# Performance work log

Hardware: AMD Instinct MI355X
Metric: run time of the kernel (lower is better)

The kernel has to match this reference:

```python
import jax, jax.numpy as jnp
import numpy as np

DEPTH = 2
DIM = 512
FF = 2048
INNER = 32
VOCAB = 8192
B = 2
L = 512
LN_EPS = 1e-5


def _layer_norm(x, g, b):
    m = jnp.mean(x, axis=-1, keepdims=True)
    v = jnp.var(x, axis=-1, keepdims=True)
    return (x - m) * jax.lax.rsqrt(v + LN_EPS) * g + b


def _sioconv_layer(x, wa, wx, v_re, v_im, h0_re, h0_im, w_ol):
    # x: [B, L, DIM] float32
    Bb, Ll, _ = x.shape
    I = v_re.shape[0]
    # complex gate a with magnitude sigmoid(log|a|^2)
    af = (x @ wa.T).reshape(Bb, Ll, I, 2)
    a = jax.lax.complex(af[..., 0], af[..., 1])
    m = jnp.square(af[..., 0]) + jnp.square(af[..., 1])
    a = a * jax.lax.rsqrt(m) * jax.nn.sigmoid(jnp.log(m))  # [B,L,I] complex
    # complex input x with magnitude |x| (x * rsqrt(|x|^2) * |x|^2)
    xf = (x @ wx.T).reshape(Bb, Ll, I, 2)
    xc = jax.lax.complex(xf[..., 0], xf[..., 1])
    mx = jnp.square(xf[..., 0]) + jnp.square(xf[..., 1])
    xc = xc * jax.lax.rsqrt(mx) * mx  # [B,L,I] complex
    # cumulative log-decay products: the original's FFT conv of the upper-
    # triangular a_ln against an all-ones matrix is exactly a cumsum along j.
    a_ln = jnp.log(a)  # [B,L,I]
    ii = jnp.arange(Ll)[:, None]
    jj = jnp.arange(Ll)[None, :]
    tri = jnp.where((jj >= ii)[None, None, :, :],
                    jnp.transpose(a_ln, (0, 2, 1))[:, :, None, :],
                    jnp.zeros((), a_ln.dtype))  # [B,I,L,L]: tri[b,d,i,j]=a_ln[b,j,d] for j>=i
    s = jnp.cumsum(tri, axis=3)
    # c[b,d,i,j] = prod_{t=i..j} a[b,t,d] for j>=i; =1 at j=i-1; 0 below.
    c = jnp.where((jj >= ii - 1)[None, None, :, :], jnp.exp(s), jnp.zeros((), s.dtype))
    V = jax.lax.complex(v_re, v_im)
    Vinv = jnp.linalg.inv(V)
    h0 = jax.lax.complex(h0_re, h0_im)  # [I]
    xct = jnp.transpose(xc, (0, 2, 1))  # [B,I,L]
    x_roll = jnp.roll(xct, 1, axis=2).at[:, :, 0].set(h0[None, :])
    # original builds C[b,l,m,n,o] = V diag(c) V^-1 then einsum; contract lazily:
    y = jnp.einsum('ko,bol->bkl', Vinv, x_roll)  # eigenbasis inputs [B,I,L]
    t = jnp.einsum('bkij,bki->bjk', c, y)        # recurrence in eigenbasis [B,L,I]
    h = jnp.einsum('bjk,nk->bjn', t, V)          # back to state basis [B,L,I]
    h = h.at[:, -1, :].add(xc[:, -1, :])         # last step input (others already in c via j=i-1 band)
    return jnp.real(h) @ w_ol.T


def setup_inputs() -> dict:
    key = jax.random.key(0)
    ks = jax.random.split(key, 16)
    f = lambda k, shp: jax.random.normal(k, shp, dtype=jnp.float32)
    return {
        'x': f(ks[0], (B, L, VOCAB)),
        'w_in': f(ks[1], (DIM, VOCAB)) * VOCAB ** -0.5,
        'b_in': jnp.zeros((DIM,), jnp.float32),
        'ln1_g': jnp.ones((DEPTH, DIM), jnp.float32),
        'ln1_b': jnp.zeros((DEPTH, DIM), jnp.float32),
        'wa': f(ks[2], (DEPTH, 2 * INNER, DIM)) * DIM ** -0.5,
        'wx': f(ks[3], (DEPTH, 2 * INNER, DIM)) * DIM ** -0.5,
        'v_re': f(ks[4], (DEPTH, INNER, INNER)),
        'v_im': f(ks[5], (DEPTH, INNER, INNER)),
        'h0_re': f(ks[6], (DEPTH, INNER)),
        'h0_im': f(ks[7], (DEPTH, INNER)),
        'w_ol': f(ks[8], (DEPTH, DIM, INNER)) * INNER ** -0.5,
        'ln2_g': jnp.ones((DEPTH, DIM), jnp.float32),
        'ln2_b': jnp.zeros((DEPTH, DIM), jnp.float32),
        'w1': f(ks[9], (DEPTH, FF, DIM)) * DIM ** -0.5,
        'b1': jnp.zeros((DEPTH, FF), jnp.float32),
        'w2': f(ks[10], (DEPTH, DIM, FF)) * FF ** -0.5,
        'b2': jnp.zeros((DEPTH, DIM), jnp.float32),
        'lnl_g': jnp.ones((DIM,), jnp.float32),
        'lnl_b': jnp.zeros((DIM,), jnp.float32),
        'w_out': f(ks[11], (VOCAB, DIM)) * DIM ** -0.5,
        'b_out': jnp.zeros((VOCAB,), jnp.float32),
    }


def reference(x, w_in, b_in, ln1_g, ln1_b, wa, wx, v_re, v_im, h0_re, h0_im,
              w_ol, ln2_g, ln2_b, w1, b1, w2, b2, lnl_g, lnl_b, w_out, b_out):
    h = x @ w_in.T + b_in  # [B,L,DIM]
    for d in range(DEPTH):
        r = h
        z = _layer_norm(h, ln1_g[d], ln1_b[d])
        z = _sioconv_layer(z, wa[d], wx[d], v_re[d], v_im[d], h0_re[d], h0_im[d], w_ol[d])
        h = z + r
        r = h
        z = _layer_norm(h, ln2_g[d], ln2_b[d])
        z = jax.nn.silu(z @ w1[d].T + b1[d]) @ w2[d].T + b2[d]
        h = z + r
    h = _layer_norm(h, lnl_g, lnl_b)
    return h @ w_out.T + b_out
```

## Files before the change

### kernel.cpp

```cpp
#include <hip/hip_runtime.h>
#include <stdint.h>

#define DEPTHC 2
#define DIMC   512
#define FFC    2048
#define INNERC 32
#define VOCABC 8192
#define BC     2
#define LC     512
#define NTOK   1024

typedef _Float16 f16;
typedef __attribute__((ext_vector_type(8))) _Float16 f16x8;
typedef __attribute__((ext_vector_type(4))) float f32x4;

__device__ __forceinline__ float2 cmul2(float2 a, float2 b){
    return make_float2(a.x*b.x - a.y*b.y, a.x*b.y + a.y*b.x);
}
__device__ __forceinline__ float2 cadd2(float2 a, float2 b){
    return make_float2(a.x + b.x, a.y + b.y);
}

__device__ __forceinline__ void gl_lds16(const void* g, void* l){
    __builtin_amdgcn_global_load_lds(
        (const __attribute__((address_space(1))) unsigned int*)g,
        (__attribute__((address_space(3))) unsigned int*)l, 16, 0, 0);
}

__global__ __launch_bounds__(256) void k_prep(
    const float* __restrict__ s0, const float* __restrict__ s1,
    const float* __restrict__ s2, const float* __restrict__ s3,
    const float* __restrict__ s4,
    f16* __restrict__ d0, f16* __restrict__ d1, f16* __restrict__ d2,
    f16* __restrict__ d3, f16* __restrict__ d4,
    int n0, int n1, int n2, int n3, int n4,
    const float* __restrict__ v_re, const float* __restrict__ v_im,
    const float* __restrict__ h0re, const float* __restrict__ h0im,
    float2* __restrict__ vinv, float2* __restrict__ h0c)
{
    __shared__ float2 M[32][64];
    if (blockIdx.x < 2){
        const int d = blockIdx.x;
        const int tid = threadIdx.x;
        const int c = tid & 63;
        const int wv = tid >> 6;
        if (tid < 32) h0c[d*32 + tid] = make_float2(h0re[d*32 + tid], h0im[d*32 + tid]);
#pragma unroll
        for (int rr = 0; rr < 8; ++rr){
            int r = wv*8 + rr;
            float re, im;
            if (c < 32){ re = v_re[d*1024 + r*32 + c]; im = v_im[d*1024 + r*32 + c]; }
            else       { re = (c - 32 == r) ? 1.f : 0.f; im = 0.f; }
            M[r][c] = make_float2(re, im);
        }
        __syncthreads();
#pragma unroll 1
        for (int col = 0; col < 32; ++col){
            float2 prow = M[col][c];
            float pvx = __shfl(prow.x, col, 64);
            float pvy = __shfl(prow.y, col, 64);
            float dm = pvx*pvx + pvy*pvy;
            float ir = pvx/dm, ii = -pvy/dm;
            float2 nv = make_float2(prow.x*ir - prow.y*ii, prow.x*ii + prow.y*ir);
#pragma unroll
            for (int rr = 0; rr < 8; ++rr){
                int r = wv*8 + rr;
                if (r == col) continue;
                float2 f  = M[r][col];
                float2 m0 = M[r][c];
                m0.x -= f.x*nv.x - f.y*nv.y;
                m0.y -= f.x*nv.y + f.y*nv.x;
                M[r][c] = m0;
            }
            __syncthreads();
        }
        if (c >= 32){
#pragma unroll
            for (int rr = 0; rr < 8; ++rr){
                int r = wv*8 + rr;
                float2 dv = M[r][r];
                float dm = dv.x*dv.x + dv.y*dv.y;
                float ir = dv.x/dm, ii = -dv.y/dm;
                float2 m0 = M[r][c];
                vinv[d*1024 + r*32 + (c - 32)] =
                    make_float2(m0.x*ir - m0.y*ii, m0.x*ii + m0.y*ir);
            }
        }
        return;
    }
    long long i = ((long long)(blockIdx.x - 2) * 256 + threadIdx.x) * 4;
    const float* s; f16* d;
    if (i < n0){ s = s0; d = d0; }
    else { i -= n0;
        if (i < n1){ s = s1; d = d1; }
        else { i -= n1;
            if (i < n2){ s = s2; d = d2; }
            else { i -= n2;
                if (i < n3){ s = s3; d = d3; }
                else { i -= n3; if (i >= n4) return; s = s4; d = d4; }
            }
        }
    }
    float4 v = *(const float4*)(s + i);
    union { f16 h[4]; float2 f2; } u;
    u.h[0] = (f16)v.x; u.h[1] = (f16)v.y; u.h[2] = (f16)v.z; u.h[3] = (f16)v.w;
    *(float2*)(d + i) = u.f2;
}

template<int MT, int NT, int MODE>
__global__ __launch_bounds__(256) void k_gemmT(
    const f16* __restrict__ A, const f16* __restrict__ Bw,
    void* __restrict__ C, const float* __restrict__ bias,
    int N, int K, int klen, int partStride)
{
    constexpr int RM = MT/32, RN = NT/32;
    __shared__ __align__(16) f16 As[MT*32];
    __shared__ __align__(16) f16 Bs[NT*32];
    const int tid = threadIdx.x;
    const int m0 = blockIdx.y * MT;
    const int n0 = blockIdx.x * NT;
    const int kbeg = blockIdx.z * klen;
    const int l = tid & 63;
    const int w = tid >> 6;
    const int fr = l & 15;
    const int fq = l >> 4;
    const int wm = (w >> 1) * (MT/2);
    const int wn = (w & 1) * (NT/2);
    const f16* gA = A  + (size_t)(m0 + (tid >> 2)) * K + kbeg + (tid & 3) * 8;
    const f16* gB = Bw + (size_t)(n0 + (tid >> 2)) * K + kbeg + (tid & 3) * 8;
    const size_t rowskip = (size_t)64 * K;
    f16* lA = As + tid * 8;
    f16* lB = Bs + tid * 8;
    f32x4 acc[RM][RN];
#pragma unroll
    for (int i = 0; i < RM; ++i)
#pragma unroll
        for (int j = 0; j < RN; ++j)
            acc[i][j] = (f32x4){0.f, 0.f, 0.f, 0.f};
    for (int kk = 0; kk < klen; kk += 32){
        __syncthreads();
#pragma unroll
        for (int i = 0; i < MT/64; ++i) gl_lds16(gA + i*rowskip, lA + i*2048);
#pragma unroll
        for (int i = 0; i < NT/64; ++i) gl_lds16(gB + i*rowskip, lB + i*2048);
        gA += 32; gB += 32;
        __syncthreads();
        f16x8 af[RM], bf[RN];
#pragma unroll
        for (int i = 0; i < RM; ++i) af[i] = *(const f16x8*)(As + (wm + 16*i + fr) * 32 + fq * 8);
#pragma unroll
        for (int j = 0; j < RN; ++j) bf[j] = *(const f16x8*)(Bs + (wn + 16*j + fr) * 32 + fq * 8);
#pragma unroll
        for (int i = 0; i < RM; ++i)
#pragma unroll
            for (int j = 0; j < RN; ++j)
                acc[i][j] = __builtin_amdgcn_mfma_f32_16x16x32_f16(af[i], bf[j], acc[i][j], 0, 0, 0);
    }
#pragma unroll
    for (int i = 0; i < RM; ++i)
#pragma unroll
        for (int j = 0; j < RN; ++j)
#pragma unroll
            for (int r = 0; r < 4; ++r){
                int row = m0 + wm + 16*i + fq*4 + r;
                int col = n0 + wn + 16*j + fr;
                if (MODE == 1){
                    ((float*)C + (size_t)blockIdx.z * partStride)[(size_t)row * N + col] = acc[i][j][r];
                } else if (MODE == 0){
                    ((float*)C)[(size_t)row * N + col] = acc[i][j][r] + bias[col];
                } else {
                    float v = acc[i][j][r] + bias[col];
                    ((f16*)C)[(size_t)row * N + col] = (f16)(v / (1.f + __expf(-v)));
                }
            }
}

__global__ __launch_bounds__(128) void k_red8_ln(
    const float* __restrict__ part, const float* __restrict__ bias,
    const float* __restrict__ res, const float* __restrict__ g,
    const float* __restrict__ b, f16* __restrict__ out, int n)
{
    int row = blockIdx.x;
    int tid = threadIdx.x;
    __shared__ float sw[2], qw[2];
    float v[4]; float s = 0.f, q = 0.f;
#pragma unroll
    for (int j = 0; j < 4; ++j){
        int c = tid + 128*j;
        int idx = row*DIMC + c;
        float t = bias[c] + res[idx];
#pragma unroll
        for (int z = 0; z < 8; ++z) t += part[(size_t)z * n + idx];
        v[j] = t; s += t; q += t*t;
    }
    for (int off = 32; off; off >>= 1){ s += __shfl_down(s, off, 64); q += __shfl_down(q, off, 64); }
    if ((tid & 63) == 0){ sw[tid >> 6] = s; qw[tid >> 6] = q; }
    __syncthreads();
    float S = sw[0] + sw[1], Q = qw[0] + qw[1];
    float m = S / DIMC;
    float rstd = rsqrtf(Q / DIMC - m*m + 1e-5f);
#pragma unroll
    for (int j = 0; j < 4; ++j){
        int c = tid + 128*j;
        out[(size_t)row*DIMC + c] = (f16)((v[j] - m)*rstd*g[c] + b[c]);
    }
}

__global__ __launch_bounds__(128) void k_siogate(
    const float* __restrict__ part, const float* __restrict__ bias,
    const float* __restrict__ res, float* __restrict__ hout,
    const float* __restrict__ g, const float* __restrict__ b,
    const float* __restrict__ wa, const float* __restrict__ wx,
    float2* __restrict__ a_t, float2* __restrict__ xc)
{
    __shared__ float zs[4][DIMC];
    __shared__ float sc[4][128];
    __shared__ float rs2[2], rq2[2];
    int tid = threadIdx.x;
    int r0 = blockIdx.x * 4;
    const int n = NTOK * DIMC;
    for (int gg = 0; gg < 4; ++gg){
        int row = r0 + gg;
        float v[4]; float s = 0.f, q = 0.f;
#pragma unroll
        for (int j = 0; j < 4; ++j){
            int c = tid + 128*j;
            int idx = row*DIMC + c;
            float t = bias[c];
            if (res) t += res[idx];
#pragma unroll
            for (int z = 0; z < 8; ++z) t += part[(size_t)z * n + idx];
            hout[idx] = t;
            v[j] = t; s += t; q += t*t;
        }
        for (int off = 32; off; off >>= 1){ s += __shfl_down(s, off, 64); q += __shfl_down(q, off, 64); }
        if ((tid & 63) == 0){ rs2[tid >> 6] = s; rq2[tid >> 6] = q; }
        __syncthreads();
        float m = (rs2[0] + rs2[1]) / DIMC;
        float var = (rq2[0] + rq2[1]) / DIMC - m*m;
        float rst = rsqrtf(var + 1e-5f);
#pragma unroll
        for (int j = 0; j < 4; ++j){ int c = tid + 128*j; zs[gg][c] = (v[j] - m)*rst*g[c] + b[c]; }
        __syncthreads();
    }
    const float* wrow = (tid < 64) ? (wa + (size_t)tid * DIMC) : (wx + (size_t)(tid - 64) * DIMC);
    float dot[4] = {0.f, 0.f, 0.f, 0.f};
    for (int c = 0; c < DIMC; c += 4){
        float4 wv = *(const float4*)(wrow + c);
#pragma unroll
        for (int gg = 0; gg < 4; ++gg){
            float4 zv = *(const float4*)(&zs[gg][c]);
            dot[gg] += wv.x*zv.x + wv.y*zv.y + wv.z*zv.z + wv.w*zv.w;
        }
    }
#pragma unroll
    for (int gg = 0; gg < 4; ++gg) sc[gg][tid] = dot[gg];
    __syncthreads();
    int gg = tid >> 5, k = tid & 31;
    int row = r0 + gg;
    int bb = row >> 9, t = row & 511;
    float re = sc[gg][2*k], im = sc[gg][2*k + 1];
    float m2 = re*re + im*im;
    float sa = rsqrtf(m2) * (m2 / (1.f + m2));
    a_t[(size_t)(bb*INNERC + k)*LC + t] = make_float2(re*sa, im*sa);
    float xr2 = sc[gg][64 + 2*k], xi2 = sc[gg][64 + 2*k + 1];
    float mx = xr2*xr2 + xi2*xi2;
    float sx = sqrtf(mx);
    xc[(size_t)row*INNERC + k] = make_float2(xr2*sx, xi2*sx);
}

__global__ __launch_bounds__(64) void k_scan(
    const float2* __restrict__ a_t, const float2* __restrict__ xc,
    const float2* __restrict__ vinv, const float2* __restrict__ h0c,
    float2* __restrict__ e)
{
    int bk = blockIdx.x;
    int l = threadIdx.x;
    int bb = bk >> 5, k = bk & 31;
    float2 vrow[32];
#pragma unroll
    for (int o = 0; o < 32; ++o) vrow[o] = vinv[k*32 + o];
    int base = bk * LC + l * 8;
    float2 av[8], wv[8];
#pragma unroll
    for (int j = 0; j < 8; ++j) av[j] = a_t[base + j];
#pragma unroll
    for (int j = 0; j < 8; ++j){
        int t = l*8 + j;
        const float2* src = (t == 0) ? h0c : (xc + (size_t)(bb*LC + t - 1) * INNERC);
        float2 acc = make_float2(0.f, 0.f);
#pragma unroll
        for (int o = 0; o < 32; o += 2){
            float4 qq = *(const float4*)(src + o);
            acc.x += vrow[o].x*qq.x - vrow[o].y*qq.y;
            acc.y += vrow[o].x*qq.y + vrow[o].y*qq.x;
            acc.x += vrow[o+1].x*qq.z - vrow[o+1].y*qq.w;
            acc.y += vrow[o+1].x*qq.w + vrow[o+1].y*qq.z;
        }
        wv[j] = acc;
    }
    float2 A = make_float2(1.f, 0.f), Bc = make_float2(0.f, 0.f);
#pragma unroll
    for (int j = 0; j < 8; ++j){
        Bc = cmul2(av[j], cadd2(Bc, wv[j]));
        A  = cmul2(av[j], A);
    }
    for (int off = 1; off < 64; off <<= 1){
        float Apx = __shfl_up(A.x,  off, 64), Apy = __shfl_up(A.y,  off, 64);
        float Bpx = __shfl_up(Bc.x, off, 64), Bpy = __shfl_up(Bc.y, off, 64);
        if (l >= off){
            float2 Ap = make_float2(Apx, Apy), Bp = make_float2(Bpx, Bpy);
            Bc = cadd2(cmul2(A, Bp), Bc);
            A  = cmul2(A, Ap);
        }
    }
    float ex = __shfl_up(Bc.x, 1, 64), ey = __shfl_up(Bc.y, 1, 64);
    float2 ecur = (l == 0) ? make_float2(0.f, 0.f) : make_float2(ex, ey);
    size_t obase = ((size_t)bb*LC + l*8) * INNERC + k;
#pragma unroll
    for (int j = 0; j < 8; ++j){
        ecur = cmul2(av[j], cadd2(ecur, wv[j]));
        e[obase + (size_t)j * INNERC] = ecur;
    }
}

__global__ __launch_bounds__(128) void k_siout_ln(
    const float2* __restrict__ e, const float2* __restrict__ xc,
    const float* __restrict__ vre, const float* __restrict__ vim,
    const float* __restrict__ wol, const float* __restrict__ res,
    const float* __restrict__ g2, const float* __restrict__ b2,
    float* __restrict__ hout, f16* __restrict__ zout)
{
    int bt = blockIdx.x;
    int tid = threadIdx.x;
    __shared__ float hr[INNERC];
    __shared__ float2 er[INNERC];
    __shared__ float sw[2], qw[2];
    if (tid < 32) er[tid] = e[(size_t)bt*INNERC + tid];
    __syncthreads();
    if (tid < 32){
        const float* vrr = vre + tid*INNERC;
        const float* vir = vim + tid*INNERC;
        float acc = xc[(size_t)bt*INNERC + tid].x;
#pragma unroll
        for (int k2 = 0; k2 < 32; ++k2) acc += vrr[k2]*er[k2].x - vir[k2]*er[k2].y;
        hr[tid] = acc;
    }
    __syncthreads();
    float v[4]; float s = 0.f, q = 0.f;
#pragma unroll
    for (int j = 0; j < 4; ++j){
        int n = tid + 128*j;
        float val = res[(size_t)bt*DIMC + n];
        const float* wr = wol + (size_t)n * INNERC;
#pragma unroll
        for (int i = 0; i < 32; ++i) val += hr[i]*wr[i];
        hout[(size_t)bt*DIMC + n] = val;
        v[j] = val; s += val; q += val*val;
    }
    for (int off = 32; off; off >>= 1){ s += __shfl_down(s, off, 64); q += __shfl_down(q, off, 64); }
    if ((tid & 63) == 0){ sw[tid >> 6] = s; qw[tid >> 6] = q; }
    __syncthreads();
    float S = sw[0] + sw[1], Q = qw[0] + qw[1];
    float m = S / DIMC;
    float rstd = rsqrtf(Q / DIMC - m*m + 1e-5f);
#pragma unroll
    for (int j = 0; j < 4; ++j){
        int n = tid + 128*j;
        zout[(size_t)bt*DIMC + n] = (f16)((v[j] - m)*rstd*g2[n] + b2[n]);
    }
}

extern "C" void kernel_launch(void* const* d_in, const int* in_sizes, int n_in,
                              void* d_out, int out_size, void* d_ws, size_t ws_size,
                              hipStream_t stream)
{
    const float* x     = (const float*)d_in[0];
    const float* w_in  = (const float*)d_in[1];
    const float* b_in  = (const float*)d_in[2];
    const float* ln1_g = (const float*)d_in[3];
    const float* ln1_b = (const float*)d_in[4];
    const float* wa    = (const float*)d_in[5];
    const float* wx    = (const float*)d_in[6];
    const float* v_re  = (const float*)d_in[7];
    const float* v_im  = (const float*)d_in[8];
    const float* h0_re = (const float*)d_in[9];
    const float* h0_im = (const float*)d_in[10];
    const float* w_ol  = (const float*)d_in[11];
    const float* ln2_g = (const float*)d_in[12];
    const float* ln2_b = (const float*)d_in[13];
    const float* w1    = (const float*)d_in[14];
    const float* b1    = (const float*)d_in[15];
    const float* w2    = (const float*)d_in[16];
    const float* b2    = (const float*)d_in[17];
    const float* lnl_g = (const float*)d_in[18];
    const float* lnl_b = (const float*)d_in[19];
    const float* w_out = (const float*)d_in[20];
    const float* b_out = (const float*)d_in[21];

    char* p = (char*)d_ws;
    f16* xb   = (f16*)p;   p += (size_t)NTOK * VOCABC * 2;
    f16* wib  = (f16*)p;   p += (size_t)DIMC * VOCABC * 2;
    f16* wob  = (f16*)p;   p += (size_t)VOCABC * DIMC * 2;
    f16* w1b  = (f16*)p;   p += (size_t)DEPTHC * FFC * DIMC * 2;
    f16* w2b  = (f16*)p;   p += (size_t)DEPTHC * DIMC * FFC * 2;
    float* h1 = (float*)p; p += (size_t)NTOK * DIMC * 4;
    float* h2 = (float*)p; p += (size_t)NTOK * DIMC * 4;
    float* h3 = (float*)p; p += (size_t)NTOK * DIMC * 4;
    f16* zb   = (f16*)p;   p += (size_t)NTOK * DIMC * 2;
    f16* ffb  = (f16*)p;   p += (size_t)NTOK * FFC * 2;
    float* pbuf = (float*)p; p += (size_t)8 * NTOK * DIMC * 4;
    float2* a_t = (float2*)p; p += (size_t)BC * INNERC * LC * 8;
    float2* xc  = (float2*)p; p += (size_t)NTOK * INNERC * 8;
    float2* ev  = (float2*)p; p += (size_t)NTOK * INNERC * 8;
    float2* vinv = (float2*)p; p += (size_t)DEPTHC * INNERC * INNERC * 8;
    float2* h0c  = (float2*)p; p += (size_t)DEPTHC * INNERC * 8;

    {
        const int n0 = NTOK*VOCABC, n1 = DIMC*VOCABC, n2 = DEPTHC*FFC*DIMC,
                  n3 = DEPTHC*DIMC*FFC, n4 = VOCABC*DIMC;
        int blocks = (n0 + n1 + n2 + n3 + n4) / 1024 + 2;
        k_prep<<<blocks, 256, 0, stream>>>(x, w_in, w1, w2, w_out,
                                           xb, wib, w1b, w2b, wob, n0, n1, n2, n3, n4,
                                           v_re, v_im, h0_re, h0_im, vinv, h0c);
    }

    {
        dim3 g(DIMC/128, NTOK/64, 8);
        k_gemmT<64,128,1><<<g, 256, 0, stream>>>(xb, wib, pbuf, nullptr, DIMC, VOCABC, VOCABC/8, NTOK*DIMC);
    }

    for (int d = 0; d < DEPTHC; ++d){
        float* cur = (d == 0) ? h1 : h3;
        float* hb  = h2;
        const float* redBias = (d == 0) ? b_in : (b2 + (d-1)*DIMC);
        const float* redRes  = (d == 0) ? nullptr : h2;
        k_siogate<<<NTOK/4, 128, 0, stream>>>(pbuf, redBias, redRes, cur,
                                              ln1_g + d*DIMC, ln1_b + d*DIMC,
                                              wa + (size_t)d*2*INNERC*DIMC,
                                              wx + (size_t)d*2*INNERC*DIMC, a_t, xc);
        k_scan<<<BC*INNERC, 64, 0, stream>>>(a_t, xc, vinv + d*INNERC*INNERC, h0c + d*INNERC, ev);
        k_siout_ln<<<NTOK, 128, 0, stream>>>(ev, xc, v_re + d*INNERC*INNERC, v_im + d*INNERC*INNERC,
                                             w_ol + (size_t)d*DIMC*INNERC, cur,
                                             ln2_g + d*DIMC, ln2_b + d*DIMC, hb, zb);
        {
            dim3 g(FFC/128, NTOK/64, 1);
            k_gemmT<64,128,2><<<g, 256, 0, stream>>>(zb, w1b + (size_t)d*FFC*DIMC, ffb, b1 + d*FFC,
                                                     FFC, DIMC, DIMC, 0);
        }
        {
            dim3 g(DIMC/128, NTOK/64, 8);
            k_gemmT<64,128,1><<<g, 256, 0, stream>>>(ffb, w2b + (size_t)d*DIMC*FFC, pbuf, nullptr,
                                                     DIMC, FFC, FFC/8, NTOK*DIMC);
        }
    }
    k_red8_ln<<<NTOK, 128, 0, stream>>>(pbuf, b2 + (DEPTHC-1)*DIMC, h2, lnl_g, lnl_b, zb, NTOK*DIMC);
    {
        dim3 g(VOCABC/128, NTOK/128, 1);
        k_gemmT<128,128,0><<<g, 256, 0, stream>>>(zb, wob, (float*)d_out, b_out, VOCABC, DIMC, DIMC, 0);
    }
    (void)in_sizes; (void)n_in; (void)out_size; (void)ws_size;
}
```

Baseline: 385.2 us.

## Store split-K partials in fp16, double GEMM K-step, split reduction from siogate

The split-K GEMM now writes its eight partial sums as fp16 instead of fp32, halving partial-buffer traffic. The GEMM main loop now loads a 64-wide K slice per barrier pair instead of 32, which halves synchronisation and doubles LDS use. The partial reduction is moved out of k_siogate into a new elementwise k_reduce8 kernel, adding one launch. Rounding each partial to fp16 before summing loses precision and can overflow in the input projection, whose K is 8192.

```diff
diff --git a/kernel.cpp b/kernel.cpp
--- a/kernel.cpp
+++ b/kernel.cpp
@@ -114,8 +114,8 @@
     int N, int K, int klen, int partStride)
 {
     constexpr int RM = MT/32, RN = NT/32;
-    __shared__ __align__(16) f16 As[MT*32];
-    __shared__ __align__(16) f16 Bs[NT*32];
+    __shared__ __align__(16) f16 As[MT*64];
+    __shared__ __align__(16) f16 Bs[NT*64];
     const int tid = threadIdx.x;
     const int m0 = blockIdx.y * MT;
     const int n0 = blockIdx.x * NT;
@@ -126,9 +126,9 @@
     const int fq = l >> 4;
     const int wm = (w >> 1) * (MT/2);
     const int wn = (w & 1) * (NT/2);
-    const f16* gA = A  + (size_t)(m0 + (tid >> 2)) * K + kbeg + (tid & 3) * 8;
-    const f16* gB = Bw + (size_t)(n0 + (tid >> 2)) * K + kbeg + (tid & 3) * 8;
-    const size_t rowskip = (size_t)64 * K;
+    const f16* gA = A  + (size_t)(m0 + (tid >> 3)) * K + kbeg + (tid & 7) * 8;
+    const f16* gB = Bw + (size_t)(n0 + (tid >> 3)) * K + kbeg + (tid & 7) * 8;
+    const size_t rowskip = (size_t)32 * K;
     f16* lA = As + tid * 8;
     f16* lB = Bs + tid * 8;
     f32x4 acc[RM][RN];
@@ -137,24 +137,27 @@
 #pragma unroll
         for (int j = 0; j < RN; ++j)
             acc[i][j] = (f32x4){0.f, 0.f, 0.f, 0.f};
-    for (int kk = 0; kk < klen; kk += 32){
+    for (int kk = 0; kk < klen; kk += 64){
         __syncthreads();
 #pragma unroll
-        for (int i = 0; i < MT/64; ++i) gl_lds16(gA + i*rowskip, lA + i*2048);
-#pragma unroll
-        for (int i = 0; i < NT/64; ++i) gl_lds16(gB + i*rowskip, lB + i*2048);
-        gA += 32; gB += 32;
+        for (int i = 0; i < MT/32; ++i) gl_lds16(gA + i*rowskip, lA + i*2048);
+#pragma unroll
+        for (int i = 0; i < NT/32; ++i) gl_lds16(gB + i*rowskip, lB + i*2048);
+        gA += 64; gB += 64;
         __syncthreads();
-        f16x8 af[RM], bf[RN];
-#pragma unroll
-        for (int i = 0; i < RM; ++i) af[i] = *(const f16x8*)(As + (wm + 16*i + fr) * 32 + fq * 8);
-#pragma unroll
-        for (int j = 0; j < RN; ++j) bf[j] = *(const f16x8*)(Bs + (wn + 16*j + fr) * 32 + fq * 8);
-#pragma unroll
-        for (int i = 0; i < RM; ++i)
-#pragma unroll
-            for (int j = 0; j < RN; ++j)
-                acc[i][j] = __builtin_amdgcn_mfma_f32_16x16x32_f16(af[i], bf[j], acc[i][j], 0, 0, 0);
+#pragma unroll
+        for (int h = 0; h < 2; ++h){
+            f16x8 af[RM], bf[RN];
+#pragma unroll
+            for (int i = 0; i < RM; ++i) af[i] = *(const f16x8*)(As + (wm + 16*i + fr) * 64 + h*32 + fq * 8);
+#pragma unroll
+            for (int j = 0; j < RN; ++j) bf[j] = *(const f16x8*)(Bs + (wn + 16*j + fr) * 64 + h*32 + fq * 8);
+#pragma unroll
+            for (int i = 0; i < RM; ++i)
+#pragma unroll
+                for (int j = 0; j < RN; ++j)
+                    acc[i][j] = __builtin_amdgcn_mfma_f32_16x16x32_f16(af[i], bf[j], acc[i][j], 0, 0, 0);
+        }
     }
 #pragma unroll
     for (int i = 0; i < RM; ++i)
@@ -165,7 +168,7 @@
                 int row = m0 + wm + 16*i + fq*4 + r;
                 int col = n0 + wn + 16*j + fr;
                 if (MODE == 1){
-                    ((float*)C + (size_t)blockIdx.z * partStride)[(size_t)row * N + col] = acc[i][j][r];
+                    ((f16*)C + (size_t)blockIdx.z * partStride)[(size_t)row * N + col] = (f16)acc[i][j][r];
                 } else if (MODE == 0){
                     ((float*)C)[(size_t)row * N + col] = acc[i][j][r] + bias[col];
                 } else {
@@ -175,8 +178,25 @@
             }
 }
 
+__global__ __launch_bounds__(256) void k_reduce8(
+    float* __restrict__ out, const f16* __restrict__ part,
+    const float* __restrict__ bias, const float* __restrict__ res, int n)
+{
+    int i = (blockIdx.x * 256 + threadIdx.x) * 2;
+    if (i >= n) return;
+    float v0 = bias[i & (DIMC - 1)], v1 = bias[(i + 1) & (DIMC - 1)];
+    if (res){ v0 += res[i]; v1 += res[i + 1]; }
+#pragma unroll
+    for (int z = 0; z < 8; ++z){
+        union { uint32_t u; f16 h[2]; } q;
+        q.u = *(const uint32_t*)(part + (size_t)z * n + i);
+        v0 += (float)q.h[0]; v1 += (float)q.h[1];
+    }
+    *(float2*)(out + i) = make_float2(v0, v1);
+}
+
 __global__ __launch_bounds__(128) void k_red8_ln(
-    const float* __restrict__ part, const float* __restrict__ bias,
+    const f16* __restrict__ part, const float* __restrict__ bias,
     const float* __restrict__ res, const float* __restrict__ g,
     const float* __restrict__ b, f16* __restrict__ out, int n)
 {
@@ -190,7 +210,7 @@
         int idx = row*DIMC + c;
         float t = bias[c] + res[idx];
 #pragma unroll
-        for (int z = 0; z < 8; ++z) t += part[(size_t)z * n + idx];
+        for (int z = 0; z < 8; ++z) t += (float)part[(size_t)z * n + idx];
         v[j] = t; s += t; q += t*t;
     }
     for (int off = 32; off; off >>= 1){ s += __shfl_down(s, off, 64); q += __shfl_down(q, off, 64); }
@@ -207,9 +227,7 @@
 }
 
 __global__ __launch_bounds__(128) void k_siogate(
-    const float* __restrict__ part, const float* __restrict__ bias,
-    const float* __restrict__ res, float* __restrict__ hout,
-    const float* __restrict__ g, const float* __restrict__ b,
+    const float* __restrict__ H, const float* __restrict__ g, const float* __restrict__ b,
     const float* __restrict__ wa, const float* __restrict__ wx,
     float2* __restrict__ a_t, float2* __restrict__ xc)
 {
@@ -218,21 +236,11 @@
     __shared__ float rs2[2], rq2[2];
     int tid = threadIdx.x;
     int r0 = blockIdx.x * 4;
-    const int n = NTOK * DIMC;
     for (int gg = 0; gg < 4; ++gg){
-        int row = r0 + gg;
+        const float* xr = H + (size_t)(r0 + gg) * DIMC;
         float v[4]; float s = 0.f, q = 0.f;
 #pragma unroll
-        for (int j = 0; j < 4; ++j){
-            int c = tid + 128*j;
-            int idx = row*DIMC + c;
-            float t = bias[c];
-            if (res) t += res[idx];
-#pragma unroll
-            for (int z = 0; z < 8; ++z) t += part[(size_t)z * n + idx];
-            hout[idx] = t;
-            v[j] = t; s += t; q += t*t;
-        }
+        for (int j = 0; j < 4; ++j){ v[j] = xr[tid + 128*j]; s += v[j]; q += v[j]*v[j]; }
         for (int off = 32; off; off >>= 1){ s += __shfl_down(s, off, 64); q += __shfl_down(q, off, 64); }
         if ((tid & 63) == 0){ rs2[tid >> 6] = s; rq2[tid >> 6] = q; }
         __syncthreads();
@@ -409,7 +417,7 @@
     float* h3 = (float*)p; p += (size_t)NTOK * DIMC * 4;
     f16* zb   = (f16*)p;   p += (size_t)NTOK * DIMC * 2;
     f16* ffb  = (f16*)p;   p += (size_t)NTOK * FFC * 2;
-    float* pbuf = (float*)p; p += (size_t)8 * NTOK * DIMC * 4;
+    f16* pbuf = (f16*)p;   p += (size_t)8 * NTOK * DIMC * 2;
     float2* a_t = (float2*)p; p += (size_t)BC * INNERC * LC * 8;
     float2* xc  = (float2*)p; p += (size_t)NTOK * INNERC * 8;
     float2* ev  = (float2*)p; p += (size_t)NTOK * INNERC * 8;
@@ -435,8 +443,8 @@
         float* hb  = h2;
         const float* redBias = (d == 0) ? b_in : (b2 + (d-1)*DIMC);
         const float* redRes  = (d == 0) ? nullptr : h2;
-        k_siogate<<<NTOK/4, 128, 0, stream>>>(pbuf, redBias, redRes, cur,
-                                              ln1_g + d*DIMC, ln1_b + d*DIMC,
+        k_reduce8<<<(NTOK*DIMC)/512, 256, 0, stream>>>(cur, pbuf, redBias, redRes, NTOK*DIMC);
+        k_siogate<<<NTOK/4, 128, 0, stream>>>(cur, ln1_g + d*DIMC, ln1_b + d*DIMC,
                                               wa + (size_t)d*2*INNERC*DIMC,
                                               wx + (size_t)d*2*INNERC*DIMC, a_t, xc);
         k_scan<<<BC*INNERC, 64, 0, stream>>>(a_t, xc, vinv + d*INNERC*INNERC, h0c + d*INNERC, ev);
```

Measured after the change: 364.8 us. 5.3% less time.
